# Kernel tuning notes

Hardware: AMD Instinct MI355X
Metric: run time of the kernel (lower is better)

The kernel has to match this reference:

```python
import jax, jax.numpy as jnp
import numpy as np

EPS = 1e-8  # torch cosine_similarity default eps


def compute_similarity(x, k, dilation=1):
    # x: [B, C, H, W]; returns [B, k*k-1, H, W] cosine similarity of each
    # pixel's channel vector vs its k x k neighborhood (center excluded).
    B, C, H, W = x.shape
    pad = (k // 2) * dilation
    # im2col: [B, C*k*k, H, W], channels ordered (C, kh, kw)
    patches = jax.lax.conv_general_dilated_patches(
        x, (k, k), (1, 1), padding=[(pad, pad), (pad, pad)],
        rhs_dilation=(dilation, dilation))
    patches = patches.reshape(B, C, k * k, H, W)
    center = patches[:, :, k * k // 2]                      # [B, C, H, W]
    dot = jnp.einsum('bchw,bcphw->bphw', center, patches)   # [B, k*k, H, W]
    n_center = jnp.sqrt(jnp.sum(center * center, axis=1))   # [B, H, W]
    n_patch = jnp.sqrt(jnp.sum(patches * patches, axis=1))  # [B, k*k, H, W]
    sim = dot / jnp.maximum(n_center[:, None] * n_patch, EPS)
    # drop the center (self-similarity == 1)
    c = k * k // 2
    return jnp.concatenate([sim[:, :c], sim[:, c + 1:]], axis=1)


def setup_inputs() -> dict:
    key = jax.random.key(0)
    x = jax.random.normal(key, (2, 128, 96, 96), dtype=jnp.float32)
    return {
        'x': x,
        'edge_threshold1': jnp.float32(0.3),
        'edge_threshold2': jnp.float32(0.3),
    }


def reference(x, edge_threshold1, edge_threshold2):
    LARGE_K, SMALL_K, DIL = 9, 5, 1
    large_sim = compute_similarity(x, LARGE_K, DIL)            # [B, 80, H, W]
    large_mask = (large_sim < edge_threshold1).astype(jnp.float32)
    large_mask = jnp.sqrt(jnp.sum(large_mask * large_mask, axis=1, keepdims=True))  # L2 norm over offsets
    x_mask = large_mask * x + x
    small_sim = compute_similarity(x_mask, SMALL_K, DIL)       # [B, 24, H, W]
    small_mask = (small_sim < edge_threshold2).astype(jnp.float32)
    small_mask = jnp.sqrt(jnp.sum(small_mask * small_mask, axis=1, keepdims=True))
    edge_map = x * small_mask + x
    return edge_map
```

## Files before the change

### kernel.cpp

```cpp
#include <hip/hip_runtime.h>

#define BN   2
#define CN   128
#define HN   96
#define WN   96
#define HW   (HN * WN)
#define NPIX (BN * HW)
#define NP4  (NPIX / 4)
#define NMAP 13
#define EPSV 1e-8f

constexpr int ODY[12] = {0, 0, 1, 1, 1, 1, 1, 2, 2, 2, 2, 2};
constexpr int ODX[12] = {1, 2, -2, -1, 0, 1, 2, -2, -1, 0, 1, 2};

__global__ void __launch_bounds__(256) k_maps(const float* __restrict__ x,
                                              float* __restrict__ D) {
    const int tx = threadIdx.x;
    const int ty = threadIdx.y;
    int p4 = blockIdx.x * 8 + tx;
    int pix = p4 * 4;
    int b = pix / HW;
    int hw = pix - b * HW;
    int h = hw / WN;
    int w = hw - h * WN;
    const float* xb = x + ((size_t)b * CN + (size_t)ty * 4) * HW + h * WN + w;

    float acc[NMAP][4];
#pragma unroll
    for (int m = 0; m < NMAP; ++m)
#pragma unroll
        for (int i = 0; i < 4; ++i) acc[m][i] = 0.f;

#pragma unroll
    for (int cc = 0; cc < 4; ++cc) {
        const float* cp = xb + (size_t)cc * HW;
        float r[3][8];
        {
            float4 a1 = *(const float4*)cp;
            float2 hi = make_float2(0.f, 0.f);
            if (w + 4 < WN) hi = *(const float2*)(cp + 4);
            r[0][0] = 0.f;  r[0][1] = 0.f;
            r[0][2] = a1.x; r[0][3] = a1.y; r[0][4] = a1.z; r[0][5] = a1.w;
            r[0][6] = hi.x; r[0][7] = hi.y;
        }
#pragma unroll
        for (int ry = 1; ry < 3; ++ry) {
            float2 lo = make_float2(0.f, 0.f);
            float4 a1 = make_float4(0.f, 0.f, 0.f, 0.f);
            float2 hi = make_float2(0.f, 0.f);
            if (h + ry < HN) {
                const float* rp = cp + ry * WN;
                if (w > 0)      lo = *(const float2*)(rp - 2);
                a1 = *(const float4*)rp;
                if (w + 4 < WN) hi = *(const float2*)(rp + 4);
            }
            r[ry][0] = lo.x; r[ry][1] = lo.y;
            r[ry][2] = a1.x; r[ry][3] = a1.y; r[ry][4] = a1.z; r[ry][5] = a1.w;
            r[ry][6] = hi.x; r[ry][7] = hi.y;
        }
#pragma unroll
        for (int i = 0; i < 4; ++i) {
            float c = r[0][2 + i];
            acc[0][i] += c * c;
#pragma unroll
            for (int j = 0; j < 12; ++j)
                acc[j + 1][i] += c * r[ODY[j]][2 + i + ODX[j]];
        }
    }

    __shared__ float4 red[16][8][17];
#pragma unroll
    for (int s = 16; s >= 1; s >>= 1) {
        if (ty >= s && ty < 2 * s) {
#pragma unroll
            for (int m = 0; m < NMAP; ++m)
                red[ty - s][tx][m] =
                    make_float4(acc[m][0], acc[m][1], acc[m][2], acc[m][3]);
        }
        __syncthreads();
        if (ty < s) {
#pragma unroll
            for (int m = 0; m < NMAP; ++m) {
                float4 v = red[ty][tx][m];
                acc[m][0] += v.x; acc[m][1] += v.y;
                acc[m][2] += v.z; acc[m][3] += v.w;
            }
        }
        __syncthreads();
    }

    if (ty == 0) {
#pragma unroll
        for (int m = 0; m < NMAP; ++m)
            *(float4*)(D + (size_t)m * NPIX + pix) =
                make_float4(acc[m][0], acc[m][1], acc[m][2], acc[m][3]);
    }
}

template<int CSPLIT>
__global__ void __launch_bounds__(64) k_maskapply(const float* __restrict__ x,
                                                  const float* __restrict__ D,
                                                  const float* __restrict__ thr2p,
                                                  float* __restrict__ out) {
    int p = blockIdx.x * blockDim.x + threadIdx.x;
    if (p >= NPIX) return;
    int cg = blockIdx.y;
    const float t2 = *thr2p;
    int b = p / HW;
    int hw = p - b * HW;
    int h = hw / WN, w = hw - h * WN;

    float nc = sqrtf(D[p]);
    int count = 0;
#pragma unroll
    for (int j = 0; j < 12; ++j) {
        const int dy = ODY[j], dx = ODX[j];
        const float* Dj = D + (size_t)(j + 1) * NPIX;
        {
            float sim = 0.f;
            if (h + dy < HN && w + dx >= 0 && w + dx < WN) {
                int q = p + dy * WN + dx;
                sim = Dj[p] / fmaxf(nc * sqrtf(D[q]), EPSV);
            }
            count += (sim < t2) ? 1 : 0;
        }
        {
            float sim = 0.f;
            if (h - dy >= 0 && w - dx >= 0 && w - dx < WN) {
                int q = p - (dy * WN + dx);
                sim = Dj[q] / fmaxf(nc * sqrtf(D[q]), EPSV);
            }
            count += (sim < t2) ? 1 : 0;
        }
    }
    float s = 1.f + sqrtf((float)count);

    constexpr int CG = CN / CSPLIT;
    const float* xp = x   + ((size_t)b * CN + (size_t)cg * CG) * HW + hw;
    float*       op = out + ((size_t)b * CN + (size_t)cg * CG) * HW + hw;
#pragma unroll
    for (int c = 0; c < CG; ++c)
        op[(size_t)c * HW] = xp[(size_t)c * HW] * s;
}

extern "C" void kernel_launch(void* const* d_in, const int* in_sizes, int n_in,
                              void* d_out, int out_size, void* d_ws, size_t ws_size,
                              hipStream_t stream) {
    const float* x    = (const float*)d_in[0];
    const float* thr2 = (const float*)d_in[2];
    float* out = (float*)d_out;

    float* D = (float*)d_ws;

    k_maps<<<dim3(NP4 / 8), dim3(8, 32), 0, stream>>>(x, D);
    k_maskapply<8><<<dim3(NPIX / 64, 8), 64, 0, stream>>>(x, D, thr2, out);
}
```

Measured before the change: 86.83 us.

## Use wave shuffles for channel reduction and vectorize mask-apply with shared scales

The reduction in k_maps now starts with cross-lane shuffles inside each 64-wide wavefront. A single shared-memory pass then combines the four waves, replacing the five-step shared-memory tree and its repeated barriers. k_maskapply now runs 256 threads per 64 pixels. The first 64 threads compute each pixel's scale into shared memory, and all threads then copy x to out with float4 loads and stores over half the channels per block. This reduces the redundant mask recomputation from eight channel splits to two and widens the memory accesses, at the cost of idle threads during the scale phase and an extra barrier.

```diff
diff --git a/kernel.cpp b/kernel.cpp
--- a/kernel.cpp
+++ b/kernel.cpp
@@ -68,79 +68,101 @@
         }
     }
 
-    __shared__ float4 red[16][8][17];
 #pragma unroll
-    for (int s = 16; s >= 1; s >>= 1) {
-        if (ty >= s && ty < 2 * s) {
+    for (int m = 0; m < NMAP; ++m)
 #pragma unroll
-            for (int m = 0; m < NMAP; ++m)
-                red[ty - s][tx][m] =
-                    make_float4(acc[m][0], acc[m][1], acc[m][2], acc[m][3]);
+        for (int i = 0; i < 4; ++i) {
+            float v = acc[m][i];
+            v += __shfl_xor(v, 8);
+            v += __shfl_xor(v, 16);
+            v += __shfl_xor(v, 32);
+            acc[m][i] = v;
         }
-        __syncthreads();
-        if (ty < s) {
+
+    constexpr int RS = 108;
+    __shared__ float4 red[4 * RS];
+    if ((ty & 7) == 0) {
+        int wv = ty >> 3;
 #pragma unroll
-            for (int m = 0; m < NMAP; ++m) {
-                float4 v = red[ty][tx][m];
-                acc[m][0] += v.x; acc[m][1] += v.y;
-                acc[m][2] += v.z; acc[m][3] += v.w;
-            }
-        }
-        __syncthreads();
+        for (int m = 0; m < NMAP; ++m)
+            red[wv * RS + tx * NMAP + m] =
+                make_float4(acc[m][0], acc[m][1], acc[m][2], acc[m][3]);
     }
-
+    __syncthreads();
     if (ty == 0) {
 #pragma unroll
-        for (int m = 0; m < NMAP; ++m)
-            *(float4*)(D + (size_t)m * NPIX + pix) =
-                make_float4(acc[m][0], acc[m][1], acc[m][2], acc[m][3]);
+        for (int m = 0; m < NMAP; ++m) {
+            float4 a = red[0 * RS + tx * NMAP + m];
+            float4 b4 = red[1 * RS + tx * NMAP + m];
+            float4 c4 = red[2 * RS + tx * NMAP + m];
+            float4 d4 = red[3 * RS + tx * NMAP + m];
+            *(float4*)(D + (size_t)m * NPIX + pix) = make_float4(
+                a.x + b4.x + c4.x + d4.x,
+                a.y + b4.y + c4.y + d4.y,
+                a.z + b4.z + c4.z + d4.z,
+                a.w + b4.w + c4.w + d4.w);
+        }
     }
 }
 
-template<int CSPLIT>
-__global__ void __launch_bounds__(64) k_maskapply(const float* __restrict__ x,
-                                                  const float* __restrict__ D,
-                                                  const float* __restrict__ thr2p,
-                                                  float* __restrict__ out) {
-    int p = blockIdx.x * blockDim.x + threadIdx.x;
-    if (p >= NPIX) return;
-    int cg = blockIdx.y;
-    const float t2 = *thr2p;
-    int b = p / HW;
-    int hw = p - b * HW;
-    int h = hw / WN, w = hw - h * WN;
+#define KCSPLIT 2
+#define KCG (CN / KCSPLIT)
+__global__ void __launch_bounds__(256) k_maskapply(const float* __restrict__ x,
+                                                   const float* __restrict__ D,
+                                                   const float* __restrict__ thr2p,
+                                                   float* __restrict__ out) {
+    const int t = threadIdx.x;
+    const int pbase = blockIdx.x * 64;
+    const int cg = blockIdx.y;
+    __shared__ __align__(16) float scale[64];
 
-    float nc = sqrtf(D[p]);
-    int count = 0;
+    if (t < 64) {
+        int p = pbase + t;
+        const float t2 = *thr2p;
+        int b = p / HW;
+        int hw = p - b * HW;
+        int h = hw / WN, w = hw - h * WN;
+
+        float nc = sqrtf(D[p]);
+        int count = 0;
 #pragma unroll
-    for (int j = 0; j < 12; ++j) {
-        const int dy = ODY[j], dx = ODX[j];
-        const float* Dj = D + (size_t)(j + 1) * NPIX;
-        {
-            float sim = 0.f;
-            if (h + dy < HN && w + dx >= 0 && w + dx < WN) {
-                int q = p + dy * WN + dx;
-                sim = Dj[p] / fmaxf(nc * sqrtf(D[q]), EPSV);
+        for (int j = 0; j < 12; ++j) {
+            const int dy = ODY[j], dx = ODX[j];
+            const float* Dj = D + (size_t)(j + 1) * NPIX;
+            {
+                float sim = 0.f;
+                if (h + dy < HN && w + dx >= 0 && w + dx < WN) {
+                    int q = p + dy * WN + dx;
+                    sim = Dj[p] / fmaxf(nc * sqrtf(D[q]), EPSV);
+                }
+                count += (sim < t2) ? 1 : 0;
             }
-            count += (sim < t2) ? 1 : 0;
+            {
+                float sim = 0.f;
+                if (h - dy >= 0 && w - dx >= 0 && w - dx < WN) {
+                    int q = p - (dy * WN + dx);
+                    sim = Dj[q] / fmaxf(nc * sqrtf(D[q]), EPSV);
+                }
+                count += (sim < t2) ? 1 : 0;
+            }
         }
-        {
-            float sim = 0.f;
-            if (h - dy >= 0 && w - dx >= 0 && w - dx < WN) {
-                int q = p - (dy * WN + dx);
-                sim = Dj[q] / fmaxf(nc * sqrtf(D[q]), EPSV);
-            }
-            count += (sim < t2) ? 1 : 0;
-        }
+        scale[t] = 1.f + sqrtf((float)count);
     }
-    float s = 1.f + sqrtf((float)count);
+    __syncthreads();
 
-    constexpr int CG = CN / CSPLIT;
-    const float* xp = x   + ((size_t)b * CN + (size_t)cg * CG) * HW + hw;
-    float*       op = out + ((size_t)b * CN + (size_t)cg * CG) * HW + hw;
+    const int g  = t & 15;
+    const int cb = t >> 4;
+    int b = pbase / HW;
+    int hwb = pbase - b * HW + 4 * g;
+    float4 s4 = *(const float4*)&scale[4 * g];
+    const size_t base0 = ((size_t)b * CN + (size_t)cg * KCG + cb) * HW + hwb;
 #pragma unroll
-    for (int c = 0; c < CG; ++c)
-        op[(size_t)c * HW] = xp[(size_t)c * HW] * s;
+    for (int k = 0; k < KCG / 16; ++k) {
+        size_t off = base0 + (size_t)k * 16 * HW;
+        float4 v = *(const float4*)(x + off);
+        v.x *= s4.x; v.y *= s4.y; v.z *= s4.z; v.w *= s4.w;
+        *(float4*)(out + off) = v;
+    }
 }
 
 extern "C" void kernel_launch(void* const* d_in, const int* in_sizes, int n_in,
@@ -153,5 +175,5 @@
     float* D = (float*)d_ws;
 
     k_maps<<<dim3(NP4 / 8), dim3(8, 32), 0, stream>>>(x, D);
-    k_maskapply<8><<<dim3(NPIX / 64, 8), 64, 0, stream>>>(x, D, thr2, out);
+    k_maskapply<<<dim3(NPIX / 64, KCSPLIT), 256, 0, stream>>>(x, D, thr2, out);
 }
```

Result: slower. 88.71 us (+2.2%).
